# Kernel tuning notes

Hardware: AMD Instinct MI355X
Metric: run time of the kernel (lower is better)

The kernel has to match this reference:

```python
import jax, jax.numpy as jnp
import numpy as np

B, S, H, P = 8, 2048, 512, 16
K = H // 2

def setup_inputs() -> dict:
    key = jax.random.key(0)
    ks = jax.random.split(key, 6)
    sc_h = 1.0 / np.sqrt(H)
    sc_k = 1.0 / np.sqrt(K)
    return {
        "hidden_state": jax.random.normal(ks[0], (B, S, H), dtype=jnp.float32),
        "head_w": jax.random.normal(ks[1], (P, H), dtype=jnp.float32) * sc_h,
        "head_b": jnp.zeros((P,), dtype=jnp.float32),
        "embeds": jax.random.normal(ks[2], (P, H), dtype=jnp.float32),
        "w1": jax.random.normal(ks[3], (P, H, K), dtype=jnp.float32) * sc_h,
        "b1": jnp.zeros((P, K), dtype=jnp.float32),
        "w2": jax.random.normal(ks[4], (P, K, H), dtype=jnp.float32) * sc_k,
        "b2": jnp.zeros((P, H), dtype=jnp.float32),
    }

def reference(hidden_state, head_w, head_b, embeds, w1, b1, w2, b2):
    # Routing: pool over seq, linear head, softmax over programs -> (B, P)
    pooled = hidden_state.mean(axis=1)                      # (B, H)
    logits = jnp.einsum("bh,ph->bp", pooled, head_w) + head_b
    probs = jax.nn.softmax(logits, axis=-1)                  # (B, P)

    # Add program embedding per expert: (P, B, S, H)
    x = hidden_state[None, :, :, :] + embeds[:, None, None, :]
    # Expert MLP: Linear(H->K), exact GELU, Linear(K->H)
    mid = jax.nn.gelu(
        jnp.einsum("pbsh,phk->pbsk", x, w1) + b1[:, None, None, :],
        approximate=False,
    )
    adapted = jnp.einsum("pbsk,pkh->pbsh", mid, w2) + b2[:, None, None, :]
    # Weighted sum over programs with per-batch probs
    out = jnp.einsum("pbsh,bp->bsh", adapted, probs)         # (B, S, H)
    return out
```

## Files before the change

### kernel.cpp

```cpp
#include <hip/hip_runtime.h>
#include <hip/hip_bf16.h>
#include <stdint.h>

#define B_ 8
#define S_ 2048
#define H_ 512
#define P_ 16
#define K_ 256
#define M_TOT (B_*S_)
#define KCAT (P_*K_)

typedef short bf8v __attribute__((ext_vector_type(8)));
typedef float f4v  __attribute__((ext_vector_type(4)));

__device__ __align__(16) unsigned short g_hidden[M_TOT*H_];
__device__ __align__(16) unsigned short g_w1t[P_*K_*H_];
__device__ __align__(16) unsigned short g_w2cat[H_*KCAT];
__device__ __align__(16) unsigned short g_mid[(size_t)M_TOT*KCAT];
__device__ float g_bias1[P_*K_];
__device__ float g_probs[B_*P_];

__device__ __forceinline__ unsigned short f2bf(float x){
  unsigned int u = __builtin_bit_cast(unsigned int, x);
  u += 0x7fffu + ((u >> 16) & 1u);
  return (unsigned short)(u >> 16);
}

__device__ __forceinline__ unsigned int pk2bf(float x, float y){
  return ((unsigned int)f2bf(y) << 16) | (unsigned int)f2bf(x);
}

__device__ __forceinline__ float gelu_prob(float x, float prob){
  float x2 = x*x;
  float t1 = 0.044715f*x;
  float u2 = fmaf(t1, x2, x);
  float e  = __expf(1.5957691216f*u2);
  float r  = __builtin_amdgcn_rcpf(e + 1.0f);
  float px = prob*x;
  return fmaf(-px, r, px);
}

__device__ __forceinline__ void gll16(const unsigned short* src, unsigned short* lds){
  __builtin_amdgcn_global_load_lds(
      (const __attribute__((address_space(1))) unsigned int*)src,
      (__attribute__((address_space(3))) unsigned int*)lds,
      16, 0, 0);
}

__global__ void cvt_pool(const float* __restrict__ hs, float* __restrict__ pooled,
                         const float* __restrict__ b1){
  if (blockIdx.x < 16){
    g_bias1[blockIdx.x*256 + threadIdx.x] = b1[blockIdx.x*256 + threadIdx.x];
  }
  const int row0 = blockIdx.x * 64;
  const int b = row0 >> 11;
  const int tx = threadIdx.x & 127, ty = threadIdx.x >> 7;
  const float4* src = (const float4*)(hs + (size_t)row0*H_) + tx;
  uint2* dst = (uint2*)g_hidden + (size_t)row0*(H_/4) + tx;
  float4 s = {0.f,0.f,0.f,0.f};
  for (int r = ty; r < 64; r += 2){
    float4 v = src[(size_t)r*128];
    s.x += v.x; s.y += v.y; s.z += v.z; s.w += v.w;
    uint2 o = { pk2bf(v.x, v.y), pk2bf(v.z, v.w) };
    dst[(size_t)r*128] = o;
  }
  __shared__ float4 red[256];
  red[threadIdx.x] = s;
  __syncthreads();
  if (ty == 0){
    float4 a = red[threadIdx.x], c = red[threadIdx.x + 128];
    atomicAdd(&pooled[b*H_ + tx*4 + 0], a.x + c.x);
    atomicAdd(&pooled[b*H_ + tx*4 + 1], a.y + c.y);
    atomicAdd(&pooled[b*H_ + tx*4 + 2], a.z + c.z);
    atomicAdd(&pooled[b*H_ + tx*4 + 3], a.w + c.w);
  }
}

__global__ void routing_kernel(const float* __restrict__ pooled,
                               const float* __restrict__ head_w,
                               const float* __restrict__ head_b){
  __shared__ float logits[B_][P_];
  int w = threadIdx.x >> 6, lane = threadIdx.x & 63;
  for (int i = 0; i < 16; ++i){
    int pair = w*16 + i; int b = pair >> 4; int p = pair & 15;
    float acc = 0.0f;
    for (int h = lane; h < H_; h += 64) acc += pooled[b*H_+h]*head_w[p*H_+h];
    for (int off=32; off; off>>=1) acc += __shfl_down(acc, off);
    if (lane==0) logits[b][p] = acc * (1.0f/S_) + head_b[p];
  }
  __syncthreads();
  if (threadIdx.x < B_){
    int b = threadIdx.x;
    float mx = -1e30f;
    #pragma unroll
    for (int p=0;p<P_;++p) mx = fmaxf(mx, logits[b][p]);
    float e[P_]; float s = 0.0f;
    #pragma unroll
    for (int p=0;p<P_;++p){ e[p] = __expf(logits[b][p]-mx); s += e[p]; }
    float inv = 1.0f/s;
    #pragma unroll
    for (int p=0;p<P_;++p) g_probs[b*P_+p] = e[p]*inv;
  }
}

__global__ void transpose_cvt_all(const float* __restrict__ w1,
                                  const float* __restrict__ w2,
                                  const float* __restrict__ embeds){
  const int tx = threadIdx.x & 31, ty = threadIdx.x >> 5;
  __shared__ float t[32][33];
  if (blockIdx.x < 2048){
    const int R = H_, C = K_;
    int p = blockIdx.x >> 7, rem = blockIdx.x & 127;
    int rt = rem >> 3, ct = rem & 7;
    const float* ip = w1 + (size_t)p*R*C + (size_t)(rt*32 + ty)*C + ct*32 + tx;
    #pragma unroll
    for (int k=0;k<4;++k) t[ty + 8*k][tx] = ip[(size_t)8*k*C];
    __syncthreads();
    unsigned short* op = g_w1t + (size_t)p*R*C + (size_t)(ct*32 + ty)*R + rt*32 + tx;
    #pragma unroll
    for (int k=0;k<4;++k) op[(size_t)8*k*R] = f2bf(t[tx][ty + 8*k]);
    if (ty == 0){
      float s = 0.0f;
      const float* ep = embeds + p*H_ + rt*32;
      #pragma unroll 8
      for (int hh=0; hh<32; ++hh) s = fmaf(ep[hh], t[hh][tx], s);
      atomicAdd(&g_bias1[p*K_ + ct*32 + tx], s);
    }
  } else {
    const int bid = blockIdx.x - 2048;
    const int R = K_, C = H_;
    int p = bid >> 7, rem = bid & 127;
    int rt = rem >> 4, ct = rem & 15;
    const float* ip = w2 + (size_t)p*R*C + (size_t)(rt*32 + ty)*C + ct*32 + tx;
    #pragma unroll
    for (int k=0;k<4;++k) t[ty + 8*k][tx] = ip[(size_t)8*k*C];
    __syncthreads();
    unsigned short* op = g_w2cat + (size_t)(ct*32 + ty)*KCAT + p*K_ + rt*32 + tx;
    #pragma unroll
    for (int k=0;k<4;++k) op[(size_t)8*k*KCAT] = f2bf(t[tx][ty + 8*k]);
  }
}


__device__ __forceinline__ void stage128(unsigned short* dst, const unsigned short* gsrc,
                                         int strideShorts, int koff, int tid){
  #pragma unroll
  for (int s = 0; s < 4; ++s){
    const int o   = (s*256 + tid)*8;
    const int row = o >> 6;
    const int ku  = (o & 63) >> 3;
    const int sku = ku ^ (row & 7);
    gll16(gsrc + (size_t)row*strideShorts + koff + sku*8, dst + o);
  }
}

__device__ __forceinline__ void kcompute(const unsigned short* Ab, const unsigned short* Bb,
    int rowA0, int rowB0, int l15, int lhi, f4v acc[4][4]){
  #pragma unroll
  for (int ksub=0; ksub<2; ++ksub){
    const int kb = ksub*64 + lhi*16;
    bf8v aF[4], bF[4];
    #pragma unroll
    for (int t=0; t<4; ++t){
      const int ra = rowA0 + t*16 + l15;
      aF[t] = *(const bf8v*)((const char*)Ab + ra*128 + (kb ^ ((ra&7)<<4)));
      const int rb = rowB0 + t*16 + l15;
      bF[t] = *(const bf8v*)((const char*)Bb + rb*128 + (kb ^ ((rb&7)<<4)));
    }
    __builtin_amdgcn_s_setprio(1);
    #pragma unroll
    for (int mt=0; mt<4; ++mt)
      #pragma unroll
      for (int nt=0; nt<4; ++nt)
        acc[mt][nt] = __builtin_amdgcn_mfma_f32_16x16x32_bf16(aF[mt], bF[nt], acc[mt][nt], 0,0,0);
    __builtin_amdgcn_s_setprio(0);
  }
}

__global__ __launch_bounds__(256, 4) void l1_kernel(){
  __shared__ __align__(16) unsigned short lds[128*136];
  const int bid = blockIdx.x;
  const int xcd = bid & 7, i = bid >> 3;
  const int n0 = (xcd*4 + (i&3)) * 128;
  const int m0 = (i >> 2) * 128;
  const int p = n0 >> 8;
  const int b = m0 >> 11;
  const int tid = threadIdx.x, w = tid >> 6, lane = tid & 63;
  const int wm = w >> 1, wn = w & 1, l15 = lane & 15, lhi = lane >> 4;
  const unsigned short* gA = g_hidden + (size_t)m0 * H_;
  const unsigned short* gB = g_w1t + (size_t)n0 * H_;

  f4v acc[4][4];
  #pragma unroll
  for (int a=0;a<4;++a)
    #pragma unroll
    for (int c=0;c<4;++c) acc[a][c] = {0.f,0.f,0.f,0.f};

  for (int kt = 0; kt < 8; ++kt){
    stage128(lds,        gA, H_, kt*64, tid);
    stage128(lds + 8192, gB, H_, kt*64, tid);
    __syncthreads();
    kcompute(lds, lds + 8192, wm*64, wn*64, l15, lhi, acc);
    __syncthreads();
  }

  const float prob = g_probs[b*P_ + p];
  #pragma unroll
  for (int nt=0; nt<4; ++nt){
    const int col = wn*64 + nt*16 + l15;
    const float bias = g_bias1[n0 + col];
    #pragma unroll
    for (int mt=0; mt<4; ++mt){
      const int r0 = wm*64 + mt*16 + lhi*4;
      unsigned int u01 = pk2bf(gelu_prob(acc[mt][nt][0] + bias, prob),
                               gelu_prob(acc[mt][nt][1] + bias, prob));
      unsigned int u23 = pk2bf(gelu_prob(acc[mt][nt][2] + bias, prob),
                               gelu_prob(acc[mt][nt][3] + bias, prob));
      lds[(r0+0)*136 + col] = (unsigned short)(u01 & 0xffffu);
      lds[(r0+1)*136 + col] = (unsigned short)(u01 >> 16);
      lds[(r0+2)*136 + col] = (unsigned short)(u23 & 0xffffu);
      lds[(r0+3)*136 + col] = (unsigned short)(u23 >> 16);
    }
  }
  __syncthreads();
  const int cc = tid & 15, rr = tid >> 4;
  #pragma unroll
  for (int pass=0; pass<8; ++pass){
    const int row = pass*16 + rr;
    bf8v vv = *(const bf8v*)&lds[row*136 + cc*8];
    *(bf8v*)&g_mid[(size_t)(m0+row)*KCAT + n0 + cc*8] = vv;
  }
}

__global__ __launch_bounds__(256, 2) void l2_kernel(float* __restrict__ out,
                                                   const float* __restrict__ b2){
  __shared__ __align__(16) unsigned short lds[4*128*64];
  const int bid = blockIdx.x;
  const int xcd = bid & 7, i = bid >> 3;
  const int n0 = (i & 3) * 128;
  const int m0 = (xcd*16 + (i >> 2)) * 128;
  const int b = m0 >> 11;
  const int tid = threadIdx.x, w = tid >> 6, lane = tid & 63;
  const int wm = w >> 1, wn = w & 1, l15 = lane & 15, lhi = lane >> 4;
  const unsigned short* gA = g_mid + (size_t)m0 * KCAT;
  const unsigned short* gB = g_w2cat + (size_t)n0 * KCAT;

  f4v acc[4][4];
  #pragma unroll
  for (int a=0;a<4;++a)
    #pragma unroll
    for (int c=0;c<4;++c) acc[a][c] = {0.f,0.f,0.f,0.f};

  stage128(lds + 0,     gA, KCAT, 0, tid);
  stage128(lds + 16384, gB, KCAT, 0, tid);
  for (int kt = 0; kt < 64; ++kt){
    const int cur = kt & 1;
    if (kt < 63){
      stage128(lds + (cur ? 0 : 8192),         gA, KCAT, (kt+1)*64, tid);
      stage128(lds + 16384 + (cur ? 0 : 8192), gB, KCAT, (kt+1)*64, tid);
      asm volatile("s_waitcnt vmcnt(8)" ::: "memory");
    } else {
      asm volatile("s_waitcnt vmcnt(0)" ::: "memory");
    }
    __builtin_amdgcn_s_barrier();
    kcompute(lds + (cur ? 8192 : 0), lds + 16384 + (cur ? 8192 : 0),
             wm*64, wn*64, l15, lhi, acc);
    __builtin_amdgcn_s_barrier();
  }

  float pr[P_];
  #pragma unroll
  for (int pp=0; pp<P_; ++pp) pr[pp] = g_probs[b*P_ + pp];
  #pragma unroll
  for (int nt=0; nt<4; ++nt){
    const int col = n0 + wn*64 + nt*16 + l15;
    float extra = 0.0f;
    #pragma unroll
    for (int pp=0; pp<P_; ++pp) extra = fmaf(pr[pp], b2[pp*H_ + col], extra);
    #pragma unroll
    for (int mt=0; mt<4; ++mt){
      #pragma unroll
      for (int j=0;j<4;++j){
        const int row = m0 + wm*64 + mt*16 + lhi*4 + j;
        out[(size_t)row*H_ + col] = acc[mt][nt][j] + extra;
      }
    }
  }
}

extern "C" void kernel_launch(void* const* d_in, const int* in_sizes, int n_in,
                              void* d_out, int out_size, void* d_ws, size_t ws_size,
                              hipStream_t stream){
  const float* hidden = (const float*)d_in[0];
  const float* head_w = (const float*)d_in[1];
  const float* head_b = (const float*)d_in[2];
  const float* embeds = (const float*)d_in[3];
  const float* w1     = (const float*)d_in[4];
  const float* b1     = (const float*)d_in[5];
  const float* w2     = (const float*)d_in[6];
  const float* b2     = (const float*)d_in[7];
  float* out = (float*)d_out;
  float* pooled = (float*)d_ws;
  (void)in_sizes; (void)n_in; (void)out_size; (void)ws_size;

  (void)hipMemsetAsync(pooled, 0, B_*H_*sizeof(float), stream);
  cvt_pool         <<<M_TOT/64, 256, 0, stream>>>(hidden, pooled, b1);
  routing_kernel   <<<1, 512, 0, stream>>>(pooled, head_w, head_b);
  transpose_cvt_all<<<4096, 256, 0, stream>>>(w1, w2, embeds);
  l1_kernel        <<<4096, 256, 0, stream>>>();
  l2_kernel        <<<512, 256, 0, stream>>>(out, b2);
}
```

Baseline: 245.8 us.

## Fold routing into pooling and shrink L2 tiles for more occupancy

The routing kernel is removed. Each pooling block now projects its partial sums onto head_w and atomically adds per-batch logits, and the softmax is recomputed inside l1 and l2. The l2 GEMM moves from 128x128 double-buffered tiles to 128x64 single-buffered tiles with 1024 blocks and higher launch bounds, to raise occupancy and load balance. The cost is dropping the prefetch pipeline in l2 and reading the A tile twice as often.

```diff
diff --git a/kernel.cpp b/kernel.cpp
--- a/kernel.cpp
+++ b/kernel.cpp
@@ -18,7 +18,6 @@
 __device__ __align__(16) unsigned short g_w2cat[H_*KCAT];
 __device__ __align__(16) unsigned short g_mid[(size_t)M_TOT*KCAT];
 __device__ float g_bias1[P_*K_];
-__device__ float g_probs[B_*P_];
 
 __device__ __forceinline__ unsigned short f2bf(float x){
   unsigned int u = __builtin_bit_cast(unsigned int, x);
@@ -47,14 +46,15 @@
       16, 0, 0);
 }
 
-__global__ void cvt_pool(const float* __restrict__ hs, float* __restrict__ pooled,
-                         const float* __restrict__ b1){
+__global__ void cvt_pool(const float* __restrict__ hs, float* __restrict__ logits,
+                         const float* __restrict__ b1, const float* __restrict__ head_w){
   if (blockIdx.x < 16){
     g_bias1[blockIdx.x*256 + threadIdx.x] = b1[blockIdx.x*256 + threadIdx.x];
   }
   const int row0 = blockIdx.x * 64;
   const int b = row0 >> 11;
-  const int tx = threadIdx.x & 127, ty = threadIdx.x >> 7;
+  const int tid = threadIdx.x;
+  const int tx = tid & 127, ty = tid >> 7;
   const float4* src = (const float4*)(hs + (size_t)row0*H_) + tx;
   uint2* dst = (uint2*)g_hidden + (size_t)row0*(H_/4) + tx;
   float4 s = {0.f,0.f,0.f,0.f};
@@ -65,41 +65,26 @@
     dst[(size_t)r*128] = o;
   }
   __shared__ float4 red[256];
-  red[threadIdx.x] = s;
+  red[tid] = s;
   __syncthreads();
   if (ty == 0){
-    float4 a = red[threadIdx.x], c = red[threadIdx.x + 128];
-    atomicAdd(&pooled[b*H_ + tx*4 + 0], a.x + c.x);
-    atomicAdd(&pooled[b*H_ + tx*4 + 1], a.y + c.y);
-    atomicAdd(&pooled[b*H_ + tx*4 + 2], a.z + c.z);
-    atomicAdd(&pooled[b*H_ + tx*4 + 3], a.w + c.w);
-  }
-}
-
-__global__ void routing_kernel(const float* __restrict__ pooled,
-                               const float* __restrict__ head_w,
-                               const float* __restrict__ head_b){
-  __shared__ float logits[B_][P_];
-  int w = threadIdx.x >> 6, lane = threadIdx.x & 63;
-  for (int i = 0; i < 16; ++i){
-    int pair = w*16 + i; int b = pair >> 4; int p = pair & 15;
-    float acc = 0.0f;
-    for (int h = lane; h < H_; h += 64) acc += pooled[b*H_+h]*head_w[p*H_+h];
-    for (int off=32; off; off>>=1) acc += __shfl_down(acc, off);
-    if (lane==0) logits[b][p] = acc * (1.0f/S_) + head_b[p];
-  }
-  __syncthreads();
-  if (threadIdx.x < B_){
-    int b = threadIdx.x;
-    float mx = -1e30f;
-    #pragma unroll
-    for (int p=0;p<P_;++p) mx = fmaxf(mx, logits[b][p]);
-    float e[P_]; float s = 0.0f;
-    #pragma unroll
-    for (int p=0;p<P_;++p){ e[p] = __expf(logits[b][p]-mx); s += e[p]; }
-    float inv = 1.0f/s;
-    #pragma unroll
-    for (int p=0;p<P_;++p) g_probs[b*P_+p] = e[p]*inv;
+    float4 a = red[tx], c = red[tx+128];
+    float4 sf = { a.x+c.x, a.y+c.y, a.z+c.z, a.w+c.w };
+    const float4* hw4 = (const float4*)head_w;
+    float lp[P_];
+    #pragma unroll
+    for (int pp=0; pp<P_; ++pp){
+      float4 hv = hw4[pp*128 + tx];
+      lp[pp] = sf.x*hv.x + sf.y*hv.y + sf.z*hv.z + sf.w*hv.w;
+    }
+    #pragma unroll
+    for (int off=32; off; off>>=1)
+      #pragma unroll
+      for (int pp=0; pp<P_; ++pp) lp[pp] += __shfl_down(lp[pp], off);
+    if ((tid & 63) == 0){
+      #pragma unroll
+      for (int pp=0; pp<P_; ++pp) atomicAdd(&logits[b*P_+pp], lp[pp]);
+    }
   }
 }
 
@@ -142,10 +127,11 @@
 }
 
 
-__device__ __forceinline__ void stage128(unsigned short* dst, const unsigned short* gsrc,
-                                         int strideShorts, int koff, int tid){
-  #pragma unroll
-  for (int s = 0; s < 4; ++s){
+template<int ROWS>
+__device__ __forceinline__ void stageR(unsigned short* dst, const unsigned short* gsrc,
+                                       int strideShorts, int koff, int tid){
+  #pragma unroll
+  for (int s = 0; s < ROWS/32; ++s){
     const int o   = (s*256 + tid)*8;
     const int row = o >> 6;
     const int ku  = (o & 63) >> 3;
@@ -177,7 +163,34 @@
   }
 }
 
-__global__ __launch_bounds__(256, 4) void l1_kernel(){
+__device__ __forceinline__ void kcompute2(const unsigned short* Ab, const unsigned short* Bb,
+    int rowA0, int rowB0, int l15, int lhi, f4v acc[4][2]){
+  #pragma unroll
+  for (int ksub=0; ksub<2; ++ksub){
+    const int kb = ksub*64 + lhi*16;
+    bf8v aF[4], bF[2];
+    #pragma unroll
+    for (int t=0; t<4; ++t){
+      const int ra = rowA0 + t*16 + l15;
+      aF[t] = *(const bf8v*)((const char*)Ab + ra*128 + (kb ^ ((ra&7)<<4)));
+    }
+    #pragma unroll
+    for (int t=0; t<2; ++t){
+      const int rb = rowB0 + t*16 + l15;
+      bF[t] = *(const bf8v*)((const char*)Bb + rb*128 + (kb ^ ((rb&7)<<4)));
+    }
+    __builtin_amdgcn_s_setprio(1);
+    #pragma unroll
+    for (int mt=0; mt<4; ++mt)
+      #pragma unroll
+      for (int nt=0; nt<2; ++nt)
+        acc[mt][nt] = __builtin_amdgcn_mfma_f32_16x16x32_bf16(aF[mt], bF[nt], acc[mt][nt], 0,0,0);
+    __builtin_amdgcn_s_setprio(0);
+  }
+}
+
+__global__ __launch_bounds__(256, 4) void l1_kernel(const float* __restrict__ logits,
+                                                   const float* __restrict__ head_b){
   __shared__ __align__(16) unsigned short lds[128*136];
   const int bid = blockIdx.x;
   const int xcd = bid & 7, i = bid >> 3;
@@ -197,14 +210,24 @@
     for (int c=0;c<4;++c) acc[a][c] = {0.f,0.f,0.f,0.f};
 
   for (int kt = 0; kt < 8; ++kt){
-    stage128(lds,        gA, H_, kt*64, tid);
-    stage128(lds + 8192, gB, H_, kt*64, tid);
+    stageR<128>(lds,        gA, H_, kt*64, tid);
+    stageR<128>(lds + 8192, gB, H_, kt*64, tid);
     __syncthreads();
     kcompute(lds, lds + 8192, wm*64, wn*64, l15, lhi, acc);
     __syncthreads();
   }
 
-  const float prob = g_probs[b*P_ + p];
+  float lg[P_], mx = -1e30f;
+  #pragma unroll
+  for (int pp=0; pp<P_; ++pp){
+    lg[pp] = logits[b*P_+pp]*(1.0f/S_) + head_b[pp];
+    mx = fmaxf(mx, lg[pp]);
+  }
+  float ssum = 0.0f;
+  #pragma unroll
+  for (int pp=0; pp<P_; ++pp){ lg[pp] = __expf(lg[pp]-mx); ssum += lg[pp]; }
+  const float prob = lg[p] * __builtin_amdgcn_rcpf(ssum);
+
   #pragma unroll
   for (int nt=0; nt<4; ++nt){
     const int col = wn*64 + nt*16 + l15;
@@ -232,51 +255,52 @@
   }
 }
 
-__global__ __launch_bounds__(256, 2) void l2_kernel(float* __restrict__ out,
-                                                   const float* __restrict__ b2){
-  __shared__ __align__(16) unsigned short lds[4*128*64];
+__global__ __launch_bounds__(256, 6) void l2_kernel(float* __restrict__ out,
+                                                   const float* __restrict__ b2,
+                                                   const float* __restrict__ logits,
+                                                   const float* __restrict__ head_b){
+  __shared__ __align__(16) unsigned short lds[(128+64)*64];
   const int bid = blockIdx.x;
   const int xcd = bid & 7, i = bid >> 3;
-  const int n0 = (i & 3) * 128;
-  const int m0 = (xcd*16 + (i >> 2)) * 128;
+  const int n0 = (i & 7) * 64;
+  const int m0 = (xcd*16 + (i >> 3)) * 128;
   const int b = m0 >> 11;
   const int tid = threadIdx.x, w = tid >> 6, lane = tid & 63;
   const int wm = w >> 1, wn = w & 1, l15 = lane & 15, lhi = lane >> 4;
   const unsigned short* gA = g_mid + (size_t)m0 * KCAT;
   const unsigned short* gB = g_w2cat + (size_t)n0 * KCAT;
 
-  f4v acc[4][4];
+  f4v acc[4][2];
   #pragma unroll
   for (int a=0;a<4;++a)
     #pragma unroll
-    for (int c=0;c<4;++c) acc[a][c] = {0.f,0.f,0.f,0.f};
-
-  stage128(lds + 0,     gA, KCAT, 0, tid);
-  stage128(lds + 16384, gB, KCAT, 0, tid);
+    for (int c=0;c<2;++c) acc[a][c] = {0.f,0.f,0.f,0.f};
+
   for (int kt = 0; kt < 64; ++kt){
-    const int cur = kt & 1;
-    if (kt < 63){
-      stage128(lds + (cur ? 0 : 8192),         gA, KCAT, (kt+1)*64, tid);
-      stage128(lds + 16384 + (cur ? 0 : 8192), gB, KCAT, (kt+1)*64, tid);
-      asm volatile("s_waitcnt vmcnt(8)" ::: "memory");
-    } else {
-      asm volatile("s_waitcnt vmcnt(0)" ::: "memory");
-    }
-    __builtin_amdgcn_s_barrier();
-    kcompute(lds + (cur ? 8192 : 0), lds + 16384 + (cur ? 8192 : 0),
-             wm*64, wn*64, l15, lhi, acc);
-    __builtin_amdgcn_s_barrier();
-  }
-
-  float pr[P_];
-  #pragma unroll
-  for (int pp=0; pp<P_; ++pp) pr[pp] = g_probs[b*P_ + pp];
-  #pragma unroll
-  for (int nt=0; nt<4; ++nt){
-    const int col = n0 + wn*64 + nt*16 + l15;
+    stageR<128>(lds,        gA, KCAT, kt*64, tid);
+    stageR<64> (lds + 8192, gB, KCAT, kt*64, tid);
+    __syncthreads();
+    kcompute2(lds, lds + 8192, wm*64, wn*32, l15, lhi, acc);
+    __syncthreads();
+  }
+
+  float lg[P_], mx = -1e30f;
+  #pragma unroll
+  for (int pp=0; pp<P_; ++pp){
+    lg[pp] = logits[b*P_+pp]*(1.0f/S_) + head_b[pp];
+    mx = fmaxf(mx, lg[pp]);
+  }
+  float ssum = 0.0f;
+  #pragma unroll
+  for (int pp=0; pp<P_; ++pp){ lg[pp] = __expf(lg[pp]-mx); ssum += lg[pp]; }
+  const float inv = __builtin_amdgcn_rcpf(ssum);
+
+  #pragma unroll
+  for (int nt=0; nt<2; ++nt){
+    const int col = n0 + wn*32 + nt*16 + l15;
     float extra = 0.0f;
     #pragma unroll
-    for (int pp=0; pp<P_; ++pp) extra = fmaf(pr[pp], b2[pp*H_ + col], extra);
+    for (int pp=0; pp<P_; ++pp) extra = fmaf(lg[pp]*inv, b2[pp*H_ + col], extra);
     #pragma unroll
     for (int mt=0; mt<4; ++mt){
       #pragma unroll
@@ -300,13 +324,12 @@
   const float* w2     = (const float*)d_in[6];
   const float* b2     = (const float*)d_in[7];
   float* out = (float*)d_out;
-  float* pooled = (float*)d_ws;
+  float* logits = (float*)d_ws;
   (void)in_sizes; (void)n_in; (void)out_size; (void)ws_size;
 
-  (void)hipMemsetAsync(pooled, 0, B_*H_*sizeof(float), stream);
-  cvt_pool         <<<M_TOT/64, 256, 0, stream>>>(hidden, pooled, b1);
-  routing_kernel   <<<1, 512, 0, stream>>>(pooled, head_w, head_b);
+  (void)hipMemsetAsync(logits, 0, B_*P_*sizeof(float), stream);
+  cvt_pool         <<<M_TOT/64, 256, 0, stream>>>(hidden, logits, b1, head_w);
   transpose_cvt_all<<<4096, 256, 0, stream>>>(w1, w2, embeds);
-  l1_kernel        <<<4096, 256, 0, stream>>>();
-  l2_kernel        <<<512, 256, 0, stream>>>(out, b2);
-}
+  l1_kernel        <<<4096, 256, 0, stream>>>(logits, head_b);
+  l2_kernel        <<<1024, 256, 0, stream>>>(out, b2, logits, head_b);
+}
```

After: 286.8 us. 1.17x slower.
